# Performance work log

Hardware: AMD Instinct MI355X
Metric: run time of the kernel (lower is better)

Reference implementation:

```python
import jax, jax.numpy as jnp
import numpy as np

N, E, D = 10000, 160000, 512


def setup_inputs() -> dict:
    key = jax.random.key(0)
    ks = jax.random.split(key, 5)
    x = jax.random.normal(ks[0], (N, D), dtype=jnp.float32)
    edge_index = jax.random.randint(ks[1], (2, E), 0, N, dtype=jnp.int32)
    W = jax.random.normal(ks[2], (D, D), dtype=jnp.float32) * (1.0 / np.sqrt(D))
    a_src = jax.random.normal(ks[3], (D,), dtype=jnp.float32) * 0.1
    a_dst = jax.random.normal(ks[4], (D,), dtype=jnp.float32) * 0.1
    bias = jnp.zeros((D,), dtype=jnp.float32)
    return {"x": x, "edge_index": edge_index, "W": W,
            "a_src": a_src, "a_dst": a_dst, "bias": bias}


def reference(x, edge_index, W, a_src, a_dst, bias):
    n = x.shape[0]
    # PyG GATConv default: add self-loops
    loops = jnp.arange(n, dtype=edge_index.dtype)
    src = jnp.concatenate([edge_index[0], loops])  # [E+N]
    dst = jnp.concatenate([edge_index[1], loops])  # [E+N]

    h = x @ W.T                                    # [N, D] linear projection
    e_src = h @ a_src                              # [N]
    e_dst = h @ a_dst                              # [N]
    e = e_src[src] + e_dst[dst]                    # [E+N]
    neg_slope = 0.2
    e = jnp.where(e > 0, e, neg_slope * e)         # leaky_relu

    # per-destination softmax (stable); self-loops guarantee non-empty segments
    m = jax.ops.segment_max(e, dst, num_segments=n)
    e = jnp.exp(e - m[dst])
    s = jax.ops.segment_sum(e, dst, num_segments=n)
    alpha = e / s[dst]                             # [E+N]

    msg = alpha[:, None] * h[src]                  # [E+N, D]
    out = jax.ops.segment_sum(msg, dst, num_segments=n) + bias  # [N, D]

    # module forward: x + elu(gat(x, edge_index))
    return x + jax.nn.elu(out)
```

## Files before the change

kernel.cpp:

```cpp
#include <hip/hip_runtime.h>
#include <hip/hip_bf16.h>

using bf16x8 = __attribute__((ext_vector_type(8))) __bf16;
using f32x4  = __attribute__((ext_vector_type(4))) float;

#define DFEAT 512
#define SLOTS 64

static __device__ __forceinline__ unsigned short f2bfbits(float f) {
    union { float f; unsigned int u; } v; v.f = f;
    unsigned int u = v.u;
    unsigned int r = (u + 0x7fffu + ((u >> 16) & 1u)) >> 16;
    return (unsigned short)r;
}

__global__ __launch_bounds__(256) void cvt_scatter_kernel(
    const float* __restrict__ x, const float* __restrict__ w,
    unsigned short* __restrict__ Xb, unsigned short* __restrict__ Wb,
    const int* __restrict__ srcv, const int* __restrict__ dstv,
    int* __restrict__ cur, int* __restrict__ slot,
    int nx4, int ntot4, int E, int T)
{
    int i = blockIdx.x * 256 + threadIdx.x;
    if (i < ntot4) {
        const float* in = (i < nx4) ? x : w;
        unsigned short* o = (i < nx4) ? Xb : Wb;
        int j = (i < nx4) ? i : i - nx4;
        float4 v = ((const float4*)in)[j];
        ushort4 u;
        u.x = f2bfbits(v.x); u.y = f2bfbits(v.y);
        u.z = f2bfbits(v.z); u.w = f2bfbits(v.w);
        ((ushort4*)o)[j] = u;
    }
    if (i < T) {
        int s, d;
        if (i < E) { s = srcv[i]; d = dstv[i]; }
        else       { s = d = i - E; }
        int pos = atomicAdd(&cur[d], 1);
        if (pos < SLOTS) slot[(size_t)d * SLOTS + pos] = s;
    }
}

__global__ __launch_bounds__(256, 4) void gemm_h_kernel(
    const unsigned short* __restrict__ X, const unsigned short* __restrict__ Wm,
    const float* __restrict__ avs, const float* __restrict__ avd,
    unsigned short* __restrict__ H, float* __restrict__ es, float* __restrict__ ed,
    int N)
{
    __shared__ unsigned short Bl[32 * 512];

    int L = blockIdx.x;
    int xcd = L & 7;
    int j   = L >> 3;
    int rpan = (j >> 4) * 8 + xcd;
    int cpan = j & 15;
    int rowPanels = (N + 127) >> 7;
    if (rpan >= rowPanels) return;
    int bm = rpan * 128;
    int bn = cpan * 32;

    int tid  = threadIdx.x;
    int wave = tid >> 6;
    int lane = tid & 63;
    int l15  = lane & 15;
    int quad = lane >> 4;

    for (int idx = tid; idx < 32 * 64; idx += 256) {
        int n = idx >> 6, c = idx & 63;
        uint4 v = *(const uint4*)(Wm + (size_t)(bn + n) * DFEAT + c * 8);
        int cs = c ^ (n & 7);
        *(uint4*)((char*)Bl + (size_t)n * 1024 + cs * 16) = v;
    }
    __syncthreads();

    int r0 = bm + wave * 32 + l15;
    int r1 = r0 + 16;
    int ra0 = r0 < N ? r0 : N - 1;
    int ra1 = r1 < N ? r1 : N - 1;
    const bf16x8* A0 = (const bf16x8*)(X + (size_t)ra0 * DFEAT);
    const bf16x8* A1 = (const bf16x8*)(X + (size_t)ra1 * DFEAT);
    const char* Bc = (const char*)Bl;
    int xorm = l15 & 7;
    int roff0 = (0 * 16 + l15) * 1024;
    int roff1 = (1 * 16 + l15) * 1024;

    f32x4 acc[2][2] = {};

    bf16x8 a0c = A0[quad],     a1c = A1[quad];
    bf16x8 a0n = A0[4 + quad], a1n = A1[4 + quad];
    bf16x8 b0, b1;
    {
        int cb = ((quad ^ xorm) * 16);
        b0 = *(const bf16x8*)(Bc + roff0 + cb);
        b1 = *(const bf16x8*)(Bc + roff1 + cb);
    }

    for (int k0 = 0; k0 < 16; ++k0) {
        int ka = ((k0 + 2 < 16 ? k0 + 2 : 15) * 4) + quad;
        bf16x8 a0f = A0[ka];
        bf16x8 a1f = A1[ka];
        int kb = ((k0 + 1 < 16 ? k0 + 1 : 15) * 4) + quad;
        int cb = (kb ^ xorm) * 16;
        bf16x8 bn0 = *(const bf16x8*)(Bc + roff0 + cb);
        bf16x8 bn1 = *(const bf16x8*)(Bc + roff1 + cb);
        acc[0][0] = __builtin_amdgcn_mfma_f32_16x16x32_bf16(a0c, b0, acc[0][0], 0, 0, 0);
        acc[1][0] = __builtin_amdgcn_mfma_f32_16x16x32_bf16(a1c, b0, acc[1][0], 0, 0, 0);
        acc[0][1] = __builtin_amdgcn_mfma_f32_16x16x32_bf16(a0c, b1, acc[0][1], 0, 0, 0);
        acc[1][1] = __builtin_amdgcn_mfma_f32_16x16x32_bf16(a1c, b1, acc[1][1], 0, 0, 0);
        a0c = a0n; a1c = a1n; a0n = a0f; a1n = a1f;
        b0 = bn0; b1 = bn1;
    }

    float as[2], ad[2];
    #pragma unroll
    for (int nt = 0; nt < 2; ++nt) {
        as[nt] = avs[bn + nt * 16 + l15];
        ad[nt] = avd[bn + nt * 16 + l15];
    }

    #pragma unroll
    for (int mt = 0; mt < 2; ++mt) {
        int rbase = bm + wave * 32 + mt * 16 + quad * 4;
        #pragma unroll
        for (int nt = 0; nt < 2; ++nt) {
            int col = bn + nt * 16 + l15;
            #pragma unroll
            for (int r = 0; r < 4; ++r) {
                int row = rbase + r;
                if (row < N) H[(size_t)row * DFEAT + col] = f2bfbits(acc[mt][nt][r]);
            }
        }
        #pragma unroll
        for (int r = 0; r < 4; ++r) {
            float ps = acc[mt][0][r] * as[0] + acc[mt][1][r] * as[1];
            float pd = acc[mt][0][r] * ad[0] + acc[mt][1][r] * ad[1];
            #pragma unroll
            for (int m = 1; m < 16; m <<= 1) {
                ps += __shfl_xor(ps, m);
                pd += __shfl_xor(pd, m);
            }
            int row = rbase + r;
            if (l15 == 0 && row < N) {
                atomicAdd(&es[row], ps);
                atomicAdd(&ed[row], pd);
            }
        }
    }
}

__global__ __launch_bounds__(256) void aggregate_kernel(
    const unsigned short* __restrict__ H, const float* __restrict__ x,
    const float* __restrict__ bias,
    const int* __restrict__ cur, const int* __restrict__ slot,
    const float* __restrict__ es, const float* __restrict__ ed,
    float* __restrict__ out, int N)
{
    int node = (blockIdx.x * 256 + threadIdx.x) >> 6;
    int lane = threadIdx.x & 63;
    if (node >= N) return;

    int k = cur[node];
    if (k > SLOTS) k = SLOTS;

    int   s = 0;
    float w = 0.f;
    if (lane < k) {
        s = slot[(size_t)node * SLOTS + lane];
        float e = es[s] + ed[node];
        e = e > 0.f ? e : 0.2f * e;
        w = __expf(e);
    }
    float denom = w;
    #pragma unroll
    for (int off = 32; off > 0; off >>= 1) denom += __shfl_xor(denom, off);
    float inv = 1.0f / denom;

    float a[8] = {};
    const unsigned short* Hl = H + lane * 8;

    auto accum = [&](int sj, float wj) {
        uint4 hv = *(const uint4*)(Hl + (size_t)sj * DFEAT);
        a[0] += wj * __uint_as_float(hv.x << 16);
        a[1] += wj * __uint_as_float(hv.x & 0xffff0000u);
        a[2] += wj * __uint_as_float(hv.y << 16);
        a[3] += wj * __uint_as_float(hv.y & 0xffff0000u);
        a[4] += wj * __uint_as_float(hv.z << 16);
        a[5] += wj * __uint_as_float(hv.z & 0xffff0000u);
        a[6] += wj * __uint_as_float(hv.w << 16);
        a[7] += wj * __uint_as_float(hv.w & 0xffff0000u);
    };

    int j = 0;
    for (; j + 3 < k; j += 4) {
        int   s0 = __shfl(s, j),     s1 = __shfl(s, j + 1);
        int   s2 = __shfl(s, j + 2), s3 = __shfl(s, j + 3);
        float w0 = __shfl(w, j),     w1 = __shfl(w, j + 1);
        float w2 = __shfl(w, j + 2), w3 = __shfl(w, j + 3);
        uint4 h0 = *(const uint4*)(Hl + (size_t)s0 * DFEAT);
        uint4 h1 = *(const uint4*)(Hl + (size_t)s1 * DFEAT);
        uint4 h2 = *(const uint4*)(Hl + (size_t)s2 * DFEAT);
        uint4 h3 = *(const uint4*)(Hl + (size_t)s3 * DFEAT);
        a[0] += w0 * __uint_as_float(h0.x << 16);
        a[1] += w0 * __uint_as_float(h0.x & 0xffff0000u);
        a[2] += w0 * __uint_as_float(h0.y << 16);
        a[3] += w0 * __uint_as_float(h0.y & 0xffff0000u);
        a[4] += w0 * __uint_as_float(h0.z << 16);
        a[5] += w0 * __uint_as_float(h0.z & 0xffff0000u);
        a[6] += w0 * __uint_as_float(h0.w << 16);
        a[7] += w0 * __uint_as_float(h0.w & 0xffff0000u);
        a[0] += w1 * __uint_as_float(h1.x << 16);
        a[1] += w1 * __uint_as_float(h1.x & 0xffff0000u);
        a[2] += w1 * __uint_as_float(h1.y << 16);
        a[3] += w1 * __uint_as_float(h1.y & 0xffff0000u);
        a[4] += w1 * __uint_as_float(h1.z << 16);
        a[5] += w1 * __uint_as_float(h1.z & 0xffff0000u);
        a[6] += w1 * __uint_as_float(h1.w << 16);
        a[7] += w1 * __uint_as_float(h1.w & 0xffff0000u);
        a[0] += w2 * __uint_as_float(h2.x << 16);
        a[1] += w2 * __uint_as_float(h2.x & 0xffff0000u);
        a[2] += w2 * __uint_as_float(h2.y << 16);
        a[3] += w2 * __uint_as_float(h2.y & 0xffff0000u);
        a[4] += w2 * __uint_as_float(h2.z << 16);
        a[5] += w2 * __uint_as_float(h2.z & 0xffff0000u);
        a[6] += w2 * __uint_as_float(h2.w << 16);
        a[7] += w2 * __uint_as_float(h2.w & 0xffff0000u);
        a[0] += w3 * __uint_as_float(h3.x << 16);
        a[1] += w3 * __uint_as_float(h3.x & 0xffff0000u);
        a[2] += w3 * __uint_as_float(h3.y << 16);
        a[3] += w3 * __uint_as_float(h3.y & 0xffff0000u);
        a[4] += w3 * __uint_as_float(h3.z << 16);
        a[5] += w3 * __uint_as_float(h3.z & 0xffff0000u);
        a[6] += w3 * __uint_as_float(h3.w << 16);
        a[7] += w3 * __uint_as_float(h3.w & 0xffff0000u);
    }
    for (; j < k; ++j) accum(__shfl(s, j), __shfl(w, j));

    int c = lane * 8;
    float4 b0 = *(const float4*)(bias + c);
    float4 b1 = *(const float4*)(bias + c + 4);
    float4 x0 = *(const float4*)(x + (size_t)node * DFEAT + c);
    float4 x1 = *(const float4*)(x + (size_t)node * DFEAT + c + 4);
    float r[8];
    r[0] = a[0] * inv + b0.x; r[1] = a[1] * inv + b0.y;
    r[2] = a[2] * inv + b0.z; r[3] = a[3] * inv + b0.w;
    r[4] = a[4] * inv + b1.x; r[5] = a[5] * inv + b1.y;
    r[6] = a[6] * inv + b1.z; r[7] = a[7] * inv + b1.w;
    #pragma unroll
    for (int i = 0; i < 8; ++i)
        r[i] = r[i] > 0.f ? r[i] : __expf(r[i]) - 1.f;
    float4 o0 = make_float4(x0.x + r[0], x0.y + r[1], x0.z + r[2], x0.w + r[3]);
    float4 o1 = make_float4(x1.x + r[4], x1.y + r[5], x1.z + r[6], x1.w + r[7]);
    *(float4*)(out + (size_t)node * DFEAT + c)     = o0;
    *(float4*)(out + (size_t)node * DFEAT + c + 4) = o1;
}

extern "C" void kernel_launch(void* const* d_in, const int* in_sizes, int n_in,
                              void* d_out, int out_size, void* d_ws, size_t ws_size,
                              hipStream_t stream)
{
    const float* x    = (const float*)d_in[0];
    const int*   edge = (const int*)d_in[1];
    const float* Wm   = (const float*)d_in[2];
    const float* avs  = (const float*)d_in[3];
    const float* avd  = (const float*)d_in[4];
    const float* bias = (const float*)d_in[5];

    const int D = DFEAT;
    const int N = in_sizes[0] / D;
    const int E = in_sizes[1] / 2;
    const int T = E + N;
    const int* srcv = edge;
    const int* dstv = edge + E;

    char* ws = (char*)d_ws;
    size_t off = 0;
    auto alloc = [&](size_t bytes) -> char* {
        char* p = ws + off;
        off += (bytes + 255) & ~(size_t)255;
        return p;
    };
    int*   cur  = (int*)alloc((size_t)N * 3 * 4);
    float* es   = (float*)(cur + N);
    float* ed   = es + N;
    int*   slot = (int*)alloc((size_t)N * SLOTS * 4);
    unsigned short* Xb = (unsigned short*)alloc((size_t)N * D * 2);
    unsigned short* Wb = (unsigned short*)alloc((size_t)D * D * 2);
    unsigned short* H  = (unsigned short*)alloc((size_t)N * D * 2);

    hipMemsetAsync(cur, 0, (size_t)N * 3 * 4, stream);

    int nx4   = (N * D) / 4;
    int ntot4 = nx4 + (D * D) / 4;
    int grid0 = (ntot4 > T ? ntot4 : T);
    cvt_scatter_kernel<<<dim3((grid0 + 255) / 256), 256, 0, stream>>>(
        x, Wm, Xb, Wb, srcv, dstv, cur, slot, nx4, ntot4, E, T);

    int rowPanels   = (N + 127) / 128;
    int rowPanels8  = ((rowPanels + 7) / 8) * 8;
    gemm_h_kernel<<<dim3(rowPanels8 * 16), 256, 0, stream>>>(
        Xb, Wb, avs, avd, H, es, ed, N);
    aggregate_kernel<<<dim3((N * 64 + 255) / 256), 256, 0, stream>>>(
        H, x, bias, cur, slot, es, ed, (float*)d_out, N);
}
```

Before: 148.0 us.

## Restructure GEMM to 64x64 tiles with double-buffered direct-to-LDS K staging

The projection GEMM moves from 128x32 tiles, which kept a full-K slab of W in shared memory and streamed A straight from global into registers, to 64x64 tiles. Both A and B are now staged per 64-wide K step into double-buffered, XOR-swizzled LDS using global_load_lds, so the next step's load overlaps the current step's MFMAs. The aim is more reuse of A, less LDS per block, and higher occupancy (launch bounds raised to 5 blocks). The cost is a barrier per K step and smaller per-wave work, with four MFMAs per wave per sub-step.

```diff
diff --git a/kernel.cpp b/kernel.cpp
--- a/kernel.cpp
+++ b/kernel.cpp
@@ -3,6 +3,7 @@
 
 using bf16x8 = __attribute__((ext_vector_type(8))) __bf16;
 using f32x4  = __attribute__((ext_vector_type(4))) float;
+typedef unsigned int u32;
 
 #define DFEAT 512
 #define SLOTS 64
@@ -12,6 +13,12 @@
     unsigned int u = v.u;
     unsigned int r = (u + 0x7fffu + ((u >> 16) & 1u)) >> 16;
     return (unsigned short)r;
+}
+
+static __device__ __forceinline__ void gload16(const unsigned short* g, unsigned short* l) {
+    __builtin_amdgcn_global_load_lds(
+        (const __attribute__((address_space(1))) u32*)g,
+        (__attribute__((address_space(3))) u32*)l, 16, 0, 0);
 }
 
 __global__ __launch_bounds__(256) void cvt_scatter_kernel(
@@ -41,23 +48,24 @@
     }
 }
 
-__global__ __launch_bounds__(256, 4) void gemm_h_kernel(
+__global__ __launch_bounds__(256, 5) void gemm_h_kernel(
     const unsigned short* __restrict__ X, const unsigned short* __restrict__ Wm,
     const float* __restrict__ avs, const float* __restrict__ avd,
     unsigned short* __restrict__ H, float* __restrict__ es, float* __restrict__ ed,
     int N)
 {
-    __shared__ unsigned short Bl[32 * 512];
+    __shared__ unsigned short Asm[2][64 * 64];
+    __shared__ unsigned short Bsm[2][64 * 64];
 
     int L = blockIdx.x;
     int xcd = L & 7;
-    int j   = L >> 3;
-    int rpan = (j >> 4) * 8 + xcd;
-    int cpan = j & 15;
-    int rowPanels = (N + 127) >> 7;
+    int q   = L >> 3;
+    int rpan = (q >> 3) * 8 + xcd;
+    int cpan = q & 7;
+    int rowPanels = (N + 63) >> 6;
     if (rpan >= rowPanels) return;
-    int bm = rpan * 128;
-    int bn = cpan * 32;
+    int bm = rpan * 64;
+    int bn = cpan * 64;
 
     int tid  = threadIdx.x;
     int wave = tid >> 6;
@@ -65,85 +73,90 @@
     int l15  = lane & 15;
     int quad = lane >> 4;
 
-    for (int idx = tid; idx < 32 * 64; idx += 256) {
-        int n = idx >> 6, c = idx & 63;
-        uint4 v = *(const uint4*)(Wm + (size_t)(bn + n) * DFEAT + c * 8);
-        int cs = c ^ (n & 7);
-        *(uint4*)((char*)Bl + (size_t)n * 1024 + cs * 16) = v;
-    }
+    int srow   = lane >> 3;
+    int schunk = (lane & 7) ^ (srow & 7);
+    int arow0 = bm + wave * 16 + srow;
+    int arow1 = arow0 + 8;
+    arow0 = arow0 < N ? arow0 : N - 1;
+    arow1 = arow1 < N ? arow1 : N - 1;
+    const unsigned short* gA0 = X  + (size_t)arow0 * DFEAT + schunk * 8;
+    const unsigned short* gA1 = X  + (size_t)arow1 * DFEAT + schunk * 8;
+    const unsigned short* gB0 = Wm + (size_t)(bn + wave * 16 + srow) * DFEAT + schunk * 8;
+    const unsigned short* gB1 = gB0 + (size_t)8 * DFEAT;
+
+    auto stage = [&](int buf, int s) {
+        int ko = s * 64;
+        gload16(gA0 + ko, &Asm[buf][(wave * 16 + 0) * 64]);
+        gload16(gA1 + ko, &Asm[buf][(wave * 16 + 8) * 64]);
+        gload16(gB0 + ko, &Bsm[buf][(wave * 16 + 0) * 64]);
+        gload16(gB1 + ko, &Bsm[buf][(wave * 16 + 8) * 64]);
+    };
+
+    f32x4 acc[4] = {};
+    int xa = l15 & 7;
+    int aoff = (wave * 16 + l15) * 128;
+
+    auto compute = [&](int buf) {
+        const char* Ab = (const char*)&Asm[buf][0];
+        const char* Bb = (const char*)&Bsm[buf][0];
+        #pragma unroll
+        for (int ks = 0; ks < 2; ++ks) {
+            int cb = ((ks * 4 + quad) ^ xa) * 16;
+            bf16x8 a  = *(const bf16x8*)(Ab + aoff + cb);
+            bf16x8 b0 = *(const bf16x8*)(Bb + (0 * 16 + l15) * 128 + cb);
+            bf16x8 b1 = *(const bf16x8*)(Bb + (1 * 16 + l15) * 128 + cb);
+            bf16x8 b2 = *(const bf16x8*)(Bb + (2 * 16 + l15) * 128 + cb);
+            bf16x8 b3 = *(const bf16x8*)(Bb + (3 * 16 + l15) * 128 + cb);
+            acc[0] = __builtin_amdgcn_mfma_f32_16x16x32_bf16(a, b0, acc[0], 0, 0, 0);
+            acc[1] = __builtin_amdgcn_mfma_f32_16x16x32_bf16(a, b1, acc[1], 0, 0, 0);
+            acc[2] = __builtin_amdgcn_mfma_f32_16x16x32_bf16(a, b2, acc[2], 0, 0, 0);
+            acc[3] = __builtin_amdgcn_mfma_f32_16x16x32_bf16(a, b3, acc[3], 0, 0, 0);
+        }
+    };
+
+    stage(0, 0);
     __syncthreads();
-
-    int r0 = bm + wave * 32 + l15;
-    int r1 = r0 + 16;
-    int ra0 = r0 < N ? r0 : N - 1;
-    int ra1 = r1 < N ? r1 : N - 1;
-    const bf16x8* A0 = (const bf16x8*)(X + (size_t)ra0 * DFEAT);
-    const bf16x8* A1 = (const bf16x8*)(X + (size_t)ra1 * DFEAT);
-    const char* Bc = (const char*)Bl;
-    int xorm = l15 & 7;
-    int roff0 = (0 * 16 + l15) * 1024;
-    int roff1 = (1 * 16 + l15) * 1024;
-
-    f32x4 acc[2][2] = {};
-
-    bf16x8 a0c = A0[quad],     a1c = A1[quad];
-    bf16x8 a0n = A0[4 + quad], a1n = A1[4 + quad];
-    bf16x8 b0, b1;
-    {
-        int cb = ((quad ^ xorm) * 16);
-        b0 = *(const bf16x8*)(Bc + roff0 + cb);
-        b1 = *(const bf16x8*)(Bc + roff1 + cb);
-    }
-
-    for (int k0 = 0; k0 < 16; ++k0) {
-        int ka = ((k0 + 2 < 16 ? k0 + 2 : 15) * 4) + quad;
-        bf16x8 a0f = A0[ka];
-        bf16x8 a1f = A1[ka];
-        int kb = ((k0 + 1 < 16 ? k0 + 1 : 15) * 4) + quad;
-        int cb = (kb ^ xorm) * 16;
-        bf16x8 bn0 = *(const bf16x8*)(Bc + roff0 + cb);
-        bf16x8 bn1 = *(const bf16x8*)(Bc + roff1 + cb);
-        acc[0][0] = __builtin_amdgcn_mfma_f32_16x16x32_bf16(a0c, b0, acc[0][0], 0, 0, 0);
-        acc[1][0] = __builtin_amdgcn_mfma_f32_16x16x32_bf16(a1c, b0, acc[1][0], 0, 0, 0);
-        acc[0][1] = __builtin_amdgcn_mfma_f32_16x16x32_bf16(a0c, b1, acc[0][1], 0, 0, 0);
-        acc[1][1] = __builtin_amdgcn_mfma_f32_16x16x32_bf16(a1c, b1, acc[1][1], 0, 0, 0);
-        a0c = a0n; a1c = a1n; a0n = a0f; a1n = a1f;
-        b0 = bn0; b1 = bn1;
-    }
-
-    float as[2], ad[2];
-    #pragma unroll
-    for (int nt = 0; nt < 2; ++nt) {
+    int buf = 0;
+    for (int s = 0; s < 7; ++s) {
+        stage(buf ^ 1, s + 1);
+        compute(buf);
+        __syncthreads();
+        buf ^= 1;
+    }
+    compute(buf);
+
+    float as[4], ad[4];
+    #pragma unroll
+    for (int nt = 0; nt < 4; ++nt) {
         as[nt] = avs[bn + nt * 16 + l15];
         ad[nt] = avd[bn + nt * 16 + l15];
     }
 
-    #pragma unroll
-    for (int mt = 0; mt < 2; ++mt) {
-        int rbase = bm + wave * 32 + mt * 16 + quad * 4;
-        #pragma unroll
-        for (int nt = 0; nt < 2; ++nt) {
-            int col = bn + nt * 16 + l15;
-            #pragma unroll
-            for (int r = 0; r < 4; ++r) {
-                int row = rbase + r;
-                if (row < N) H[(size_t)row * DFEAT + col] = f2bfbits(acc[mt][nt][r]);
-            }
-        }
+    int rbase = bm + wave * 16 + quad * 4;
+    #pragma unroll
+    for (int nt = 0; nt < 4; ++nt) {
+        int col = bn + nt * 16 + l15;
         #pragma unroll
         for (int r = 0; r < 4; ++r) {
-            float ps = acc[mt][0][r] * as[0] + acc[mt][1][r] * as[1];
-            float pd = acc[mt][0][r] * ad[0] + acc[mt][1][r] * ad[1];
-            #pragma unroll
-            for (int m = 1; m < 16; m <<= 1) {
-                ps += __shfl_xor(ps, m);
-                pd += __shfl_xor(pd, m);
-            }
             int row = rbase + r;
-            if (l15 == 0 && row < N) {
-                atomicAdd(&es[row], ps);
-                atomicAdd(&ed[row], pd);
-            }
+            if (row < N) H[(size_t)row * DFEAT + col] = f2bfbits(acc[nt][r]);
+        }
+    }
+    #pragma unroll
+    for (int r = 0; r < 4; ++r) {
+        float ps = acc[0][r] * as[0] + acc[1][r] * as[1]
+                 + acc[2][r] * as[2] + acc[3][r] * as[3];
+        float pd = acc[0][r] * ad[0] + acc[1][r] * ad[1]
+                 + acc[2][r] * ad[2] + acc[3][r] * ad[3];
+        #pragma unroll
+        for (int m = 1; m < 16; m <<= 1) {
+            ps += __shfl_xor(ps, m);
+            pd += __shfl_xor(pd, m);
+        }
+        int row = rbase + r;
+        if (l15 == 0 && row < N) {
+            atomicAdd(&es[row], ps);
+            atomicAdd(&ed[row], pd);
         }
     }
 }
@@ -295,9 +308,9 @@
     cvt_scatter_kernel<<<dim3((grid0 + 255) / 256), 256, 0, stream>>>(
         x, Wm, Xb, Wb, srcv, dstv, cur, slot, nx4, ntot4, E, T);
 
-    int rowPanels   = (N + 127) / 128;
-    int rowPanels8  = ((rowPanels + 7) / 8) * 8;
-    gemm_h_kernel<<<dim3(rowPanels8 * 16), 256, 0, stream>>>(
+    int rowPanels  = (N + 63) / 64;
+    int rowPanels8 = ((rowPanels + 7) / 8) * 8;
+    gemm_h_kernel<<<dim3(rowPanels8 * 8), 256, 0, stream>>>(
         Xb, Wb, avs, avd, H, es, ed, N);
     aggregate_kernel<<<dim3((N * 64 + 255) / 256), 256, 0, stream>>>(
         H, x, bias, cur, slot, es, ed, (float*)d_out, N);
```

After: 135.6 us. 1.09x faster.
